# Performance work log

Measured on AMD Instinct MI355X. Metric: run time of the kernel, lower is better.

The kernel has to match this reference:

```python
import jax, jax.numpy as jnp
import numpy as np

EMBED_DIM = 768
NUM_HEADS = 12
HEAD_DIM = EMBED_DIM // NUM_HEADS


def setup_inputs() -> dict:
    key = jax.random.key(0)
    k_x, k_wqkv, k_bqkv, k_wo, k_bo = jax.random.split(key, 5)
    B, S = 2, 4096
    x = jax.random.normal(k_x, (B, S, EMBED_DIM), dtype=jnp.float32)
    # nn.Linear default init: U(-1/sqrt(fan_in), 1/sqrt(fan_in))
    bound = 1.0 / np.sqrt(EMBED_DIM)
    w_qkv = jax.random.uniform(k_wqkv, (EMBED_DIM, 3 * EMBED_DIM), jnp.float32, -bound, bound)
    b_qkv = jax.random.uniform(k_bqkv, (3 * EMBED_DIM,), jnp.float32, -bound, bound)
    w_out = jax.random.uniform(k_wo, (EMBED_DIM, EMBED_DIM), jnp.float32, -bound, bound)
    b_out = jax.random.uniform(k_bo, (EMBED_DIM,), jnp.float32, -bound, bound)
    return {"x": x, "w_qkv": w_qkv, "b_qkv": b_qkv, "w_out": w_out, "b_out": b_out}


def reference(x, w_qkv, b_qkv, w_out, b_out):
    B, S, E = x.shape
    H, D = NUM_HEADS, HEAD_DIM
    qkv = x @ w_qkv + b_qkv                       # [B,S,3E]
    qkv = qkv.reshape(B, S, 3, H, D)
    q = qkv[:, :, 0].transpose(0, 2, 1, 3)        # [B,H,S,D]
    k = qkv[:, :, 1].transpose(0, 2, 1, 3)
    v = qkv[:, :, 2].transpose(0, 2, 1, 3)
    scores = jnp.einsum('bhqd,bhkd->bhqk', q, k) / jnp.sqrt(jnp.float32(D))
    causal = jnp.tril(jnp.ones((S, S), dtype=bool))
    scores = jnp.where(causal, scores, -jnp.inf)
    weights = jax.nn.softmax(scores, axis=-1)
    attended = jnp.einsum('bhqk,bhkd->bhqd', weights, v)  # [B,H,S,D]
    attended = attended.transpose(0, 2, 1, 3).reshape(B, S, E)
    return attended @ w_out + b_out
```

## Files before the change

kernel.cpp:

```cpp
#include <hip/hip_runtime.h>

#define EMBED 768
#define NH 12
#define HD 64
#define SEQ 4096
#define BATCH 2
#define MROWS (BATCH * SEQ)
#define N3E (3 * EMBED)

typedef short bf16x8 __attribute__((ext_vector_type(8)));
typedef float fx4 __attribute__((ext_vector_type(4)));
typedef float f32x16 __attribute__((ext_vector_type(16)));
typedef unsigned short ushort_t;
typedef unsigned short us4 __attribute__((ext_vector_type(4)));

#if __has_builtin(__builtin_amdgcn_exp2f)
#define EXP2F(x) __builtin_amdgcn_exp2f(x)
#else
#define EXP2F(x) exp2f(x)
#endif

#define QSCALE 0.18033688011112042f

__device__ inline ushort_t f2bf(float f) {
  union { float f; unsigned int u; } x; x.f = f;
  unsigned int r = x.u + 0x7fffu + ((x.u >> 16) & 1u);
  return (ushort_t)(r >> 16);
}

__device__ inline unsigned int cvtpk(float a, float b) {
  unsigned int r;
  asm("v_cvt_pk_bf16_f32 %0, %1, %2" : "=v"(r) : "v"(a), "v"(b));
  return r;
}
__device__ inline void plswap(unsigned int& x, unsigned int& y) {
  asm("v_permlane32_swap_b32 %0, %1" : "+v"(x), "+v"(y));
}

__global__ __launch_bounds__(256) void convert_x(const float* __restrict__ in,
                                                 ushort_t* __restrict__ out) {
  int i = (blockIdx.x * 256 + threadIdx.x) * 8;
  float4 a = *(const float4*)(in + i);
  float4 b = *(const float4*)(in + i + 4);
  bf16x8 o;
  o[0] = f2bf(a.x); o[1] = f2bf(a.y); o[2] = f2bf(a.z); o[3] = f2bf(a.w);
  o[4] = f2bf(b.x); o[5] = f2bf(b.y); o[6] = f2bf(b.z); o[7] = f2bf(b.w);
  *(bf16x8*)(out + i) = o;
}

__global__ __launch_bounds__(256) void transpose_w(const float* __restrict__ in,
                                                   ushort_t* __restrict__ out,
                                                   int K, int N) {
  __shared__ float t[64][65];
  const int bn = blockIdx.x * 64, bk = blockIdx.y * 64;
  const int c = threadIdx.x & 63, r0 = threadIdx.x >> 6;
#pragma unroll
  for (int rr = 0; rr < 16; ++rr) {
    int row = rr * 4 + r0;
    t[row][c] = in[(size_t)(bk + row) * N + bn + c];
  }
  __syncthreads();
#pragma unroll
  for (int rr = 0; rr < 16; ++rr) {
    int row = rr * 4 + r0;
    out[(size_t)(bn + row) * K + bk + c] = f2bf(t[c][row]);
  }
}

template <int N_, int K_, bool SCATTER>
__global__ __launch_bounds__(256) void gemm_mfma(
    const ushort_t* __restrict__ A, const ushort_t* __restrict__ Bt,
    const float* __restrict__ bias, float* __restrict__ outF,
    ushort_t* __restrict__ oq, ushort_t* __restrict__ ok,
    ushort_t* __restrict__ ov) {
  constexpr int NT = K_ / 32;
  __shared__ __align__(16) ushort_t smem[24576];
  ushort_t* As_ = smem;
  ushort_t* Bs_ = smem + 12288;
  const int tid = threadIdx.x;
  const int w = tid >> 6, lane = tid & 63;
  const int quad = lane >> 4, ln = lane & 15;

  const int gx = gridDim.x;
  const int nwg = gx * gridDim.y;
  int lin = blockIdx.y * gx + blockIdx.x;
  lin = (lin & 7) * (nwg >> 3) + (lin >> 3);
  const int bm = (lin / gx) * 128, bn = (lin % gx) * 128;

  const int wm = (w >> 1) * 64, wn = (w & 1) * 64;
  const int sr = lane >> 2;
  const int sslot = lane & 3;

  auto STAGE = [&](int ti, int b) {
#pragma unroll
    for (int r = 0; r < 2; ++r) {
      const int c = w + r * 4;
      const int m = c * 16 + sr;
      const int kk = ti * 32 + ((sslot ^ (m & 3)) << 3);
      __builtin_amdgcn_global_load_lds(
          (const __attribute__((address_space(1))) unsigned int*)
              (A + (size_t)(bm + m) * K_ + kk),
          (__attribute__((address_space(3))) unsigned int*)(As_ + b * 4096 + c * 512),
          16, 0, 0);
      __builtin_amdgcn_global_load_lds(
          (const __attribute__((address_space(1))) unsigned int*)
              (Bt + (size_t)(bn + m) * K_ + kk),
          (__attribute__((address_space(3))) unsigned int*)(Bs_ + b * 4096 + c * 512),
          16, 0, 0);
    }
  };

  fx4 acc[4][4] = {};

  auto COMPUTE = [&](int b) {
    bf16x8 af[4], bfr[4];
#pragma unroll
    for (int i = 0; i < 4; ++i) {
      const int m = wm + i * 16 + ln;
      af[i] = *(const bf16x8*)(As_ + b * 4096 + m * 32 + ((quad ^ (m & 3)) << 3));
    }
#pragma unroll
    for (int j = 0; j < 4; ++j) {
      const int n = wn + j * 16 + ln;
      bfr[j] = *(const bf16x8*)(Bs_ + b * 4096 + n * 32 + ((quad ^ (n & 3)) << 3));
    }
#pragma unroll
    for (int i = 0; i < 4; ++i)
#pragma unroll
      for (int j = 0; j < 4; ++j)
        acc[i][j] = __builtin_amdgcn_mfma_f32_16x16x32_bf16(af[i], bfr[j],
                                                            acc[i][j], 0, 0, 0);
  };

  STAGE(0, 0);
  STAGE(1, 1);

  int bufR = 0;
  for (int t = 0; t < NT - 2; ++t) {
    asm volatile("s_waitcnt vmcnt(4)" ::: "memory");
    __builtin_amdgcn_s_barrier();
    __builtin_amdgcn_sched_barrier(0);
    const int bufS = (bufR >= 1) ? bufR - 1 : 2;
    STAGE(t + 2, bufS);
    COMPUTE(bufR);
    bufR = (bufR < 2) ? bufR + 1 : 0;
  }
  asm volatile("s_waitcnt vmcnt(4)" ::: "memory");
  __builtin_amdgcn_s_barrier();
  __builtin_amdgcn_sched_barrier(0);
  COMPUTE(bufR);
  bufR = (bufR < 2) ? bufR + 1 : 0;
  asm volatile("s_waitcnt vmcnt(0)" ::: "memory");
  __builtin_amdgcn_s_barrier();
  __builtin_amdgcn_sched_barrier(0);
  COMPUTE(bufR);

  if (!SCATTER) {
#pragma unroll
    for (int j = 0; j < 4; ++j) {
      const int n = bn + wn + j * 16 + ln;
      const float bv = bias[n];
#pragma unroll
      for (int i = 0; i < 4; ++i) {
        const int m0 = bm + wm + i * 16 + quad * 4;
#pragma unroll
        for (int r = 0; r < 4; ++r)
          outF[(size_t)(m0 + r) * N_ + n] = acc[i][j][r] + bv;
      }
    }
  } else {
    const int t3 = bn / EMBED;
    if (t3 == 2) {
      __syncthreads();
#pragma unroll
      for (int j = 0; j < 4; ++j) {
        const int nl = wn + j * 16 + ln;
        const float bv = bias[bn + nl];
        const int key = (nl & 7) << 4;
#pragma unroll
        for (int i = 0; i < 4; ++i) {
          const int m0 = wm + i * 16 + quad * 4;
#pragma unroll
          for (int r = 0; r < 4; ++r)
            smem[nl * 128 + ((m0 + r) ^ key)] = f2bf(acc[i][j][r] + bv);
        }
      }
      __syncthreads();
      const int b_ = bm >> 12, s0 = bm & 4095;
      const int lr = lane >> 4;
      const int lc = lane & 15;
#pragma unroll
      for (int it = 0; it < 8; ++it) {
        const int nl = w * 32 + it * 4 + lr;
        const int rem = bn + nl - 2 * EMBED;
        const int h = rem >> 6, d = rem & 63;
        const int mc = lc * 8;
        bf16x8 val =
            *(const bf16x8*)&smem[nl * 128 + (mc ^ ((nl & 7) << 4))];
        *(bf16x8*)&ov[((size_t)(b_ * NH + h) * HD + d) * SEQ + s0 + mc] = val;
      }
    } else {
#pragma unroll
      for (int j = 0; j < 4; ++j) {
        const int nn = bn + wn + j * 16 + ln;
        const int rem = nn - t3 * EMBED;
        const int h = rem >> 6, d = rem & 63;
        const float bv = bias[nn];
#pragma unroll
        for (int i = 0; i < 4; ++i) {
          const int m0 = bm + wm + i * 16 + quad * 4;
#pragma unroll
          for (int r = 0; r < 4; ++r) {
            const int m = m0 + r;
            const int b_ = m >> 12, s = m & 4095;
            const float v = acc[i][j][r] + bv;
            if (t3 == 0)
              oq[((size_t)(b_ * NH + h) * SEQ + s) * HD + d] = f2bf(v * QSCALE);
            else
              ok[((size_t)(b_ * NH + h) * SEQ + s) * HD + d] = f2bf(v);
          }
        }
      }
    }
  }
}

__global__ __launch_bounds__(256, 3) void flash_mfma(
    const ushort_t* __restrict__ qb, const ushort_t* __restrict__ kb,
    const ushort_t* __restrict__ vb, ushort_t* __restrict__ attn) {
  __shared__ __align__(16) ushort_t smemAll[16896];

  const int tid = threadIdx.x;
  const int w = tid >> 6;
  const int lane = tid & 63;
  const int r32 = lane & 31;
  const int hf = lane >> 5;
  const int gk = r32 & 7;
  const int rc4 = hf * 4;
  const int qh = w & 1;
  const int kh = w >> 1;

  const int bh = blockIdx.x;
  const int y = blockIdx.y;
  const int qt2 = (y < 11) ? (31 - y) : (y - 11);
  const int ktd0 = 2 * qt2;
  const int nkt = 2 * qt2 + 2;

  const size_t base = (size_t)bh * SEQ * HD;
  const ushort_t* Qg = qb + base;
  const ushort_t* Kg = kb + base;
  const ushort_t* Vg = vb + base;

  const int srow = lane >> 3;
  const int sg = (lane & 7) ^ srow;
  const int row0 = w * 8 + srow;
  const ushort_t* kp = Kg + (size_t)row0 * HD + (sg << 3);
  const ushort_t* vp = Vg + (size_t)row0 * SEQ + (sg << 3);

  const int qbase = qt2 * 128 + qh * 64 + r32;
  bf16x8 qfA[4], qfB[4];
  {
    const ushort_t* qra = Qg + (size_t)qbase * HD;
    const ushort_t* qrb = qra + (size_t)32 * HD;
#pragma unroll
    for (int dc = 0; dc < 4; ++dc) {
      qfA[dc] = *(const bf16x8*)(qra + dc * 16 + hf * 8);
      qfB[dc] = *(const bf16x8*)(qrb + dc * 16 + hf * 8);
    }
  }

  f32x16 oacc[2][2] = {};
  float lsumA = 0.f, lsumB = 0.f;

#pragma unroll
  for (int r2 = 0; r2 < 2; ++r2) {
    __builtin_amdgcn_global_load_lds(
        (const __attribute__((address_space(1))) unsigned int*)(kp + r2 * (32 * HD)),
        (__attribute__((address_space(3))) unsigned int*)(smemAll + (w + r2 * 4) * 512),
        16, 0, 0);
    __builtin_amdgcn_global_load_lds(
        (const __attribute__((address_space(1))) unsigned int*)(vp + r2 * (32 * SEQ)),
        (__attribute__((address_space(3))) unsigned int*)(smemAll + 8192 + (w + r2 * 4) * 512),
        16, 0, 0);
  }
  kp += 64 * HD;
  vp += 64;

  for (int kt = 0; kt < nkt; ++kt) {
    const int cur = kt & 1;
    __syncthreads();
    if (kt + 1 < nkt) {
      const int nxt = cur ^ 1;
#pragma unroll
      for (int r2 = 0; r2 < 2; ++r2) {
        __builtin_amdgcn_global_load_lds(
            (const __attribute__((address_space(1))) unsigned int*)(kp + r2 * (32 * HD)),
            (__attribute__((address_space(3))) unsigned int*)(smemAll + nxt * 4096 + (w + r2 * 4) * 512),
            16, 0, 0);
        __builtin_amdgcn_global_load_lds(
            (const __attribute__((address_space(1))) unsigned int*)(vp + r2 * (32 * SEQ)),
            (__attribute__((address_space(3))) unsigned int*)(smemAll + 8192 + nxt * 4096 + (w + r2 * 4) * 512),
            16, 0, 0);
      }
      kp += 64 * HD;
      vp += 64;
    }

    int rel = -64;
    if (kt >= ktd0) rel = (kt - ktd0) * 64 + kh * 32 - qh * 64;
    if (rel >= 64) continue;

    const ushort_t* Kc = smemAll + cur * 4096;
    const ushort_t* Vc = smemAll + 8192 + cur * 4096;
    const int krow = (kh * 32 + r32) * 64;

    f32x16 sA = {}, sB = {};
#pragma unroll
    for (int dc = 0; dc < 4; ++dc) {
      bf16x8 kf = *(const bf16x8*)(Kc + krow + (((2 * dc + hf) ^ gk) << 3));
      sA = __builtin_amdgcn_mfma_f32_32x32x16_bf16(kf, qfA[dc], sA, 0, 0, 0);
      sB = __builtin_amdgcn_mfma_f32_32x32x16_bf16(kf, qfB[dc], sB, 0, 0, 0);
    }
    if (rel == 0) {
#pragma unroll
      for (int r = 0; r < 16; ++r) {
        const int rowc = (r & 3) + 8 * (r >> 2) + rc4;
        if (rowc > r32) sA[r] = -1e30f;
      }
    } else if (rel == 32) {
#pragma unroll
      for (int r = 0; r < 16; ++r) {
        const int rowc = (r & 3) + 8 * (r >> 2) + rc4;
        sA[r] = -1e30f;
        if (rowc > r32) sB[r] = -1e30f;
      }
    }
    float eA[16], eB[16];
#pragma unroll
    for (int r = 0; r < 16; ++r) {
      eA[r] = EXP2F(sA[r]);
      eB[r] = EXP2F(sB[r]);
    }
    {
      float a0 = ((eA[0] + eA[1]) + (eA[2] + eA[3])) +
                 ((eA[4] + eA[5]) + (eA[6] + eA[7]));
      float a1 = ((eA[8] + eA[9]) + (eA[10] + eA[11])) +
                 ((eA[12] + eA[13]) + (eA[14] + eA[15]));
      lsumA += a0 + a1;
      float b0 = ((eB[0] + eB[1]) + (eB[2] + eB[3])) +
                 ((eB[4] + eB[5]) + (eB[6] + eB[7]));
      float b1 = ((eB[8] + eB[9]) + (eB[10] + eB[11])) +
                 ((eB[12] + eB[13]) + (eB[14] + eB[15]));
      lsumB += b0 + b1;
    }
    __builtin_amdgcn_s_setprio(1);
#pragma unroll
    for (int ch = 0; ch < 2; ++ch) {
      const int rb = ch * 8;
      unsigned int ax0 = cvtpk(eA[rb + 0], eA[rb + 1]);
      unsigned int ax1 = cvtpk(eA[rb + 2], eA[rb + 3]);
      unsigned int ay0 = cvtpk(eA[rb + 4], eA[rb + 5]);
      unsigned int ay1 = cvtpk(eA[rb + 6], eA[rb + 7]);
      plswap(ax0, ay0);
      plswap(ax1, ay1);
      union { unsigned int u[4]; bf16x8 v; } pfA;
      pfA.u[0] = ax0; pfA.u[1] = ax1; pfA.u[2] = ay0; pfA.u[3] = ay1;
      unsigned int bx0 = cvtpk(eB[rb + 0], eB[rb + 1]);
      unsigned int bx1 = cvtpk(eB[rb + 2], eB[rb + 3]);
      unsigned int by0 = cvtpk(eB[rb + 4], eB[rb + 5]);
      unsigned int by1 = cvtpk(eB[rb + 6], eB[rb + 7]);
      plswap(bx0, by0);
      plswap(bx1, by1);
      union { unsigned int u[4]; bf16x8 v; } pfB;
      pfB.u[0] = bx0; pfB.u[1] = bx1; pfB.u[2] = by0; pfB.u[3] = by1;
      const int c = kh * 2 + ch;
#pragma unroll
      for (int vb2 = 0; vb2 < 2; ++vb2) {
        bf16x8 vf = *(const bf16x8*)(Vc + (vb2 * 32 + r32) * 64 +
                                     (((2 * c + hf) ^ gk) << 3));
        oacc[0][vb2] =
            __builtin_amdgcn_mfma_f32_32x32x16_bf16(vf, pfA.v, oacc[0][vb2], 0, 0, 0);
        oacc[1][vb2] =
            __builtin_amdgcn_mfma_f32_32x32x16_bf16(vf, pfB.v, oacc[1][vb2], 0, 0, 0);
      }
    }
    __builtin_amdgcn_s_setprio(0);
  }

  lsumA += __shfl_xor(lsumA, 32);
  lsumB += __shfl_xor(lsumB, 32);
  __syncthreads();
  float* ored = (float*)smemAll;
  float* lred = (float*)(smemAll + 16384);
  if (kh == 1) {
    float* ob = ored + qh * 4096;
#pragma unroll
    for (int qc = 0; qc < 2; ++qc)
#pragma unroll
      for (int vb2 = 0; vb2 < 2; ++vb2)
#pragma unroll
        for (int r = 0; r < 16; ++r)
          ob[((qc * 2 + vb2) * 16 + r) * 64 + lane] = oacc[qc][vb2][r];
    lred[qh * 128 + lane] = lsumA;
    lred[qh * 128 + 64 + lane] = lsumB;
  }
  __syncthreads();
  if (kh == 0) {
    float* ob = ored + qh * 4096;
#pragma unroll
    for (int qc = 0; qc < 2; ++qc)
#pragma unroll
      for (int vb2 = 0; vb2 < 2; ++vb2)
#pragma unroll
        for (int r = 0; r < 16; ++r)
          oacc[qc][vb2][r] += ob[((qc * 2 + vb2) * 16 + r) * 64 + lane];
    lsumA += lred[qh * 128 + lane];
    lsumB += lred[qh * 128 + 64 + lane];
    const int b_ = bh / NH, h = bh % NH;
#pragma unroll
    for (int qc = 0; qc < 2; ++qc) {
      const float inv = 1.f / (qc ? lsumB : lsumA);
      ushort_t* orow = attn +
          (size_t)(b_ * SEQ + qt2 * 128 + qh * 64 + qc * 32 + r32) * EMBED +
          h * HD;
#pragma unroll
      for (int vb2 = 0; vb2 < 2; ++vb2)
#pragma unroll
        for (int rq = 0; rq < 4; ++rq) {
          us4 o;
#pragma unroll
          for (int r = 0; r < 4; ++r)
            o[r] = f2bf(oacc[qc][vb2][rq * 4 + r] * inv);
          *(us4*)(orow + vb2 * 32 + rq * 8 + rc4) = o;
        }
    }
  }
}

extern "C" void kernel_launch(void* const* d_in, const int* in_sizes, int n_in,
                              void* d_out, int out_size, void* d_ws,
                              size_t ws_size, hipStream_t stream) {
  const float* x = (const float*)d_in[0];
  const float* w_qkv = (const float*)d_in[1];
  const float* b_qkv = (const float*)d_in[2];
  const float* w_out = (const float*)d_in[3];
  const float* b_out = (const float*)d_in[4];
  float* out = (float*)d_out;

  const size_t per = (size_t)BATCH * NH * SEQ * HD;
  ushort_t* q_buf = (ushort_t*)d_ws;
  ushort_t* k_buf = q_buf + per;
  ushort_t* v_buf = k_buf + per;
  ushort_t* attn_buf = v_buf + per;
  ushort_t* xb = attn_buf + per;
  ushort_t* wqkvT = xb + per;
  ushort_t* woutT = wqkvT + (size_t)N3E * EMBED;

  convert_x<<<(MROWS * EMBED) / 2048, 256, 0, stream>>>(x, xb);
  transpose_w<<<dim3(N3E / 64, EMBED / 64), 256, 0, stream>>>(w_qkv, wqkvT,
                                                              EMBED, N3E);
  transpose_w<<<dim3(EMBED / 64, EMBED / 64), 256, 0, stream>>>(w_out, woutT,
                                                                EMBED, EMBED);

  dim3 g1(N3E / 128, MROWS / 128);
  gemm_mfma<N3E, EMBED, true><<<g1, 256, 0, stream>>>(
      xb, wqkvT, b_qkv, nullptr, q_buf, k_buf, v_buf);

  dim3 g2(BATCH * NH, 32);
  flash_mfma<<<g2, 256, 0, stream>>>(q_buf, k_buf, v_buf, attn_buf);

  dim3 g3(EMBED / 128, MROWS / 128);
  gemm_mfma<EMBED, EMBED, false><<<g3, 256, 0, stream>>>(
      attn_buf, woutT, b_out, out, nullptr, nullptr, nullptr);
}
```

Baseline: 223.0 us.

## Merge prep kernels into one launch and simplify GEMM to single-buffered loop

Combines the x conversion and both weight transposes into a single prep kernel dispatched by block index, which removes two kernel launches. The GEMM's triple-buffered global_load_lds pipeline is replaced with a single-buffered load/sync/compute loop, and shared memory per block shrinks from 48 KB to 32 KB. That loses overlap of loads with MFMA work and adds a barrier per k-step, in exchange for simpler code and possibly more resident blocks. Note that smem stays at 16384 elements while Bs_ now starts at offset 4096, so the B tile uses only part of it.

```diff
diff --git a/kernel.cpp b/kernel.cpp
--- a/kernel.cpp
+++ b/kernel.cpp
@@ -37,22 +37,35 @@
   asm("v_permlane32_swap_b32 %0, %1" : "+v"(x), "+v"(y));
 }
 
-__global__ __launch_bounds__(256) void convert_x(const float* __restrict__ in,
-                                                 ushort_t* __restrict__ out) {
-  int i = (blockIdx.x * 256 + threadIdx.x) * 8;
-  float4 a = *(const float4*)(in + i);
-  float4 b = *(const float4*)(in + i + 4);
-  bf16x8 o;
-  o[0] = f2bf(a.x); o[1] = f2bf(a.y); o[2] = f2bf(a.z); o[3] = f2bf(a.w);
-  o[4] = f2bf(b.x); o[5] = f2bf(b.y); o[6] = f2bf(b.z); o[7] = f2bf(b.w);
-  *(bf16x8*)(out + i) = o;
-}
-
-__global__ __launch_bounds__(256) void transpose_w(const float* __restrict__ in,
-                                                   ushort_t* __restrict__ out,
-                                                   int K, int N) {
+__global__ __launch_bounds__(256) void prep(
+    const float* __restrict__ x, ushort_t* __restrict__ xb,
+    const float* __restrict__ w_qkv, ushort_t* __restrict__ wqkvT,
+    const float* __restrict__ w_out, ushort_t* __restrict__ woutT) {
+  const int id = blockIdx.x;
+  if (id < 3072) {
+    int i = (id * 256 + threadIdx.x) * 8;
+    float4 a = *(const float4*)(x + i);
+    float4 b = *(const float4*)(x + i + 4);
+    bf16x8 o;
+    o[0] = f2bf(a.x); o[1] = f2bf(a.y); o[2] = f2bf(a.z); o[3] = f2bf(a.w);
+    o[4] = f2bf(b.x); o[5] = f2bf(b.y); o[6] = f2bf(b.z); o[7] = f2bf(b.w);
+    *(bf16x8*)(xb + i) = o;
+    return;
+  }
   __shared__ float t[64][65];
-  const int bn = blockIdx.x * 64, bk = blockIdx.y * 64;
+  const float* in;
+  ushort_t* out;
+  int N, bn, bk;
+  if (id < 3504) {
+    const int r = id - 3072;
+    in = w_qkv; out = wqkvT; N = N3E;
+    bn = (r % 36) * 64; bk = (r / 36) * 64;
+  } else {
+    const int r = id - 3504;
+    in = w_out; out = woutT; N = EMBED;
+    bn = (r % 12) * 64; bk = (r / 12) * 64;
+  }
+  const int K = EMBED;
   const int c = threadIdx.x & 63, r0 = threadIdx.x >> 6;
 #pragma unroll
   for (int rr = 0; rr < 16; ++rr) {
@@ -74,9 +87,9 @@
     ushort_t* __restrict__ oq, ushort_t* __restrict__ ok,
     ushort_t* __restrict__ ov) {
   constexpr int NT = K_ / 32;
-  __shared__ __align__(16) ushort_t smem[24576];
+  __shared__ __align__(16) ushort_t smem[16384];
   ushort_t* As_ = smem;
-  ushort_t* Bs_ = smem + 12288;
+  ushort_t* Bs_ = smem + 4096;
   const int tid = threadIdx.x;
   const int w = tid >> 6, lane = tid & 63;
   const int quad = lane >> 4, ln = lane & 15;
@@ -91,38 +104,38 @@
   const int sr = lane >> 2;
   const int sslot = lane & 3;
 
-  auto STAGE = [&](int ti, int b) {
+  fx4 acc[4][4] = {};
+
+  for (int t = 0; t < NT; ++t) {
+    __syncthreads();
 #pragma unroll
     for (int r = 0; r < 2; ++r) {
       const int c = w + r * 4;
       const int m = c * 16 + sr;
-      const int kk = ti * 32 + ((sslot ^ (m & 3)) << 3);
+      const int kk = t * 32 + ((sslot ^ (m & 3)) << 3);
       __builtin_amdgcn_global_load_lds(
           (const __attribute__((address_space(1))) unsigned int*)
               (A + (size_t)(bm + m) * K_ + kk),
-          (__attribute__((address_space(3))) unsigned int*)(As_ + b * 4096 + c * 512),
+          (__attribute__((address_space(3))) unsigned int*)(As_ + c * 512),
           16, 0, 0);
       __builtin_amdgcn_global_load_lds(
           (const __attribute__((address_space(1))) unsigned int*)
               (Bt + (size_t)(bn + m) * K_ + kk),
-          (__attribute__((address_space(3))) unsigned int*)(Bs_ + b * 4096 + c * 512),
+          (__attribute__((address_space(3))) unsigned int*)(Bs_ + c * 512),
           16, 0, 0);
     }
-  };
-
-  fx4 acc[4][4] = {};
-
-  auto COMPUTE = [&](int b) {
+    __syncthreads();
+
     bf16x8 af[4], bfr[4];
 #pragma unroll
     for (int i = 0; i < 4; ++i) {
       const int m = wm + i * 16 + ln;
-      af[i] = *(const bf16x8*)(As_ + b * 4096 + m * 32 + ((quad ^ (m & 3)) << 3));
+      af[i] = *(const bf16x8*)(As_ + m * 32 + ((quad ^ (m & 3)) << 3));
     }
 #pragma unroll
     for (int j = 0; j < 4; ++j) {
       const int n = wn + j * 16 + ln;
-      bfr[j] = *(const bf16x8*)(Bs_ + b * 4096 + n * 32 + ((quad ^ (n & 3)) << 3));
+      bfr[j] = *(const bf16x8*)(Bs_ + n * 32 + ((quad ^ (n & 3)) << 3));
     }
 #pragma unroll
     for (int i = 0; i < 4; ++i)
@@ -130,30 +143,7 @@
       for (int j = 0; j < 4; ++j)
         acc[i][j] = __builtin_amdgcn_mfma_f32_16x16x32_bf16(af[i], bfr[j],
                                                             acc[i][j], 0, 0, 0);
-  };
-
-  STAGE(0, 0);
-  STAGE(1, 1);
-
-  int bufR = 0;
-  for (int t = 0; t < NT - 2; ++t) {
-    asm volatile("s_waitcnt vmcnt(4)" ::: "memory");
-    __builtin_amdgcn_s_barrier();
-    __builtin_amdgcn_sched_barrier(0);
-    const int bufS = (bufR >= 1) ? bufR - 1 : 2;
-    STAGE(t + 2, bufS);
-    COMPUTE(bufR);
-    bufR = (bufR < 2) ? bufR + 1 : 0;
-  }
-  asm volatile("s_waitcnt vmcnt(4)" ::: "memory");
-  __builtin_amdgcn_s_barrier();
-  __builtin_amdgcn_sched_barrier(0);
-  COMPUTE(bufR);
-  bufR = (bufR < 2) ? bufR + 1 : 0;
-  asm volatile("s_waitcnt vmcnt(0)" ::: "memory");
-  __builtin_amdgcn_s_barrier();
-  __builtin_amdgcn_sched_barrier(0);
-  COMPUTE(bufR);
+  }
 
   if (!SCATTER) {
 #pragma unroll
@@ -456,11 +446,7 @@
   ushort_t* wqkvT = xb + per;
   ushort_t* woutT = wqkvT + (size_t)N3E * EMBED;
 
-  convert_x<<<(MROWS * EMBED) / 2048, 256, 0, stream>>>(x, xb);
-  transpose_w<<<dim3(N3E / 64, EMBED / 64), 256, 0, stream>>>(w_qkv, wqkvT,
-                                                              EMBED, N3E);
-  transpose_w<<<dim3(EMBED / 64, EMBED / 64), 256, 0, stream>>>(w_out, woutT,
-                                                                EMBED, EMBED);
+  prep<<<3648, 256, 0, stream>>>(x, xb, w_qkv, wqkvT, w_out, woutT);
 
   dim3 g1(N3E / 128, MROWS / 128);
   gemm_mfma<N3E, EMBED, true><<<g1, 256, 0, stream>>>(
```

Result: slower. 231.0 us (+3.6%).
